# Optimization experiments

Hardware: AMD Instinct MI355X
Metric: run time of the kernel (lower is better)

Reference implementation:

```python
import jax, jax.numpy as jnp
import numpy as np

N = 50000
E = 1600000
IN_DIM = 128
OUT_DIM = 128
HEADS = 4
C = OUT_DIM // HEADS  # per-head channels = 32
EDGE_DIM = 16
NEG_SLOPE = 0.2
LN_EPS = 1e-5


def setup_inputs() -> dict:
    key = jax.random.key(0)
    ks = jax.random.split(key, 12)
    s = 1.0 / np.sqrt(IN_DIM)
    return {
        "x": jax.random.normal(ks[0], (N, IN_DIM), dtype=jnp.float32),
        "edge_index": jax.random.randint(ks[1], (2, E), 0, N, dtype=jnp.int64),
        "edge_attr": jax.random.normal(ks[2], (E, EDGE_DIM), dtype=jnp.float32),
        # GATv2Conv params
        "W_l": jax.random.normal(ks[3], (IN_DIM, HEADS * C), dtype=jnp.float32) * s,
        "b_l": jnp.zeros((HEADS * C,), dtype=jnp.float32),
        "W_r": jax.random.normal(ks[4], (IN_DIM, HEADS * C), dtype=jnp.float32) * s,
        "b_r": jnp.zeros((HEADS * C,), dtype=jnp.float32),
        "W_e": jax.random.normal(ks[5], (EDGE_DIM, HEADS * C), dtype=jnp.float32) * (1.0 / np.sqrt(EDGE_DIM)),
        "att": jax.random.normal(ks[6], (HEADS, C), dtype=jnp.float32) * (1.0 / np.sqrt(C)),
        "conv_bias": jnp.zeros((HEADS * C,), dtype=jnp.float32),
        # LayerNorm params
        "gamma": jnp.ones((OUT_DIM,), dtype=jnp.float32),
        "beta": jnp.zeros((OUT_DIM,), dtype=jnp.float32),
    }


def _gat_layer(x, edge_index, edge_attr, W_l, b_l, W_r, b_r, W_e, att, conv_bias, gamma, beta):
    src, dst = edge_index[0], edge_index[1]
    # linear projections -> [N, H, C] / [E, H, C]
    x_l = (x @ W_l + b_l).reshape(N, HEADS, C)  # source-side
    x_r = (x @ W_r + b_r).reshape(N, HEADS, C)  # target-side
    e_f = (edge_attr @ W_e).reshape(E, HEADS, C)
    # GATv2 attention logits per edge/head
    z = x_l[src] + x_r[dst] + e_f                      # [E, H, C]
    z = jnp.where(z >= 0, z, NEG_SLOPE * z)            # LeakyReLU(0.2)
    logits = jnp.einsum('ehc,hc->eh', z, att)          # [E, H]
    # segment softmax over incoming edges of each target node
    m = jax.ops.segment_max(logits, dst, num_segments=N)          # [N, H]
    m = jnp.where(jnp.isfinite(m), m, 0.0)
    ex = jnp.exp(logits - m[dst])                                  # [E, H]
    denom = jax.ops.segment_sum(ex, dst, num_segments=N)          # [N, H]
    alpha = ex / (denom[dst] + 1e-16)                              # [E, H]
    # weighted message aggregation (dropout on alpha skipped: eval mode)
    msg = x_l[src] * alpha[:, :, None]                             # [E, H, C]
    out = jax.ops.segment_sum(msg, dst, num_segments=N)           # [N, H, C]
    out = out.reshape(N, HEADS * C) + conv_bias                    # concat heads
    # LayerNorm -> ReLU -> (dropout: identity) -> residual (Identity since in==out)
    mu = jnp.mean(out, axis=-1, keepdims=True)
    var = jnp.mean(jnp.square(out - mu), axis=-1, keepdims=True)
    out = (out - mu) * jax.lax.rsqrt(var + LN_EPS) * gamma + beta
    out = jax.nn.relu(out)
    return out + x


def reference(x, edge_index, edge_attr, W_l, b_l, W_r, b_r, W_e, att, conv_bias, gamma, beta):
    return _gat_layer(x, edge_index, edge_attr, W_l, b_l, W_r, b_r, W_e, att, conv_bias, gamma, beta)
```

## Files before the change

kernel.cpp:

```cpp
#include <hip/hip_runtime.h>
#include <hip/hip_bf16.h>

#define NPB 16
#define EPB 256

__device__ __forceinline__ float b2f(__hip_bfloat16 v) { return __bfloat162float(v); }
__device__ __forceinline__ float ldf(const void* p, long i, int f32) {
    return f32 ? ((const float*)p)[i] : b2f(((const __hip_bfloat16*)p)[i]);
}
__device__ __forceinline__ float bflo(unsigned u) { union { unsigned i; float f; } v; v.i = u << 16; return v.f; }
__device__ __forceinline__ float bfhi(unsigned u) { union { unsigned i; float f; } v; v.i = u & 0xffff0000u; return v.f; }
__device__ __forceinline__ float2 ldf2(const void* p, long i2, int f32) {
    if (f32) return ((const float2*)p)[i2];
    unsigned u = ((const unsigned*)p)[i2];
    return make_float2(bflo(u), bfhi(u));
}
__device__ __forceinline__ int ldi(const int* p, long i, int i32) {
    return i32 ? p[i] : p[2 * i];
}

template <int CTRL>
__device__ __forceinline__ float dpp_add(float v) {
    int s = __builtin_amdgcn_update_dpp(0, __float_as_int(v), CTRL, 0xF, 0xF, true);
    return v + __int_as_float(s);
}

__global__ void zero_i(int* __restrict__ a, long n, int* __restrict__ dt)
{
    long i = (long)blockIdx.x * 256 + threadIdx.x;
    long stride = (long)gridDim.x * 256;
    for (; i < n; i += stride) a[i] = 0;
    if (blockIdx.x == 0 && threadIdx.x == 0 && dt) { dt[0] = 0; dt[1] = 0; }
}

__global__ void fail_stamp(float* __restrict__ out, float code)
{
    if (threadIdx.x == 0 && blockIdx.x == 0) out[0] = code;
}

__global__ void detect_kernel(const void* __restrict__ x, const int* __restrict__ ei,
                              int* __restrict__ dt, int E_)
{
    int t = threadIdx.x;
    const unsigned short* xb = (const unsigned short*)x;
    int f32 = 0;
    for (int i = t; i < 4096; i += 256) {
        int ex = (xb[i] >> 7) & 0xFF;
        if (ex > 140) f32 = 1;
    }
    if (f32) atomicOr(&dt[0], 1);
    int nz = 0;
    for (int i = t; i < 2048; i += 256) nz |= ei[2 * i + 1];
    if (nz) atomicOr(&dt[1], 1);
}

__global__ __launch_bounds__(128) void gemm_xlr(
    const void* __restrict__ x,
    const void* __restrict__ Wl, const void* __restrict__ bl,
    const void* __restrict__ Wr, const void* __restrict__ br,
    const int* __restrict__ dt,
    __hip_bfloat16* __restrict__ xl, __hip_bfloat16* __restrict__ xr, int n)
{
    __shared__ float xs[NPB][128];
    int f32 = dt[0];
    int t = threadIdx.x;
    int n0 = blockIdx.x * NPB;
    for (int j = 0; j < NPB; ++j) {
        int node = n0 + j;
        xs[j][t] = (node < n) ? ldf(x, (long)node * 128 + t, f32) : 0.f;
    }
    __syncthreads();
    float accl[NPB], accr[NPB];
#pragma unroll
    for (int j = 0; j < NPB; ++j) { accl[j] = 0.f; accr[j] = 0.f; }
    for (int k = 0; k < 128; ++k) {
        float wl = ldf(Wl, k * 128 + t, f32);
        float wr = ldf(Wr, k * 128 + t, f32);
#pragma unroll
        for (int j = 0; j < NPB; ++j) {
            float xv = xs[j][k];
            accl[j] = fmaf(xv, wl, accl[j]);
            accr[j] = fmaf(xv, wr, accr[j]);
        }
    }
    float blv = ldf(bl, t, f32);
    float brv = ldf(br, t, f32);
    for (int j = 0; j < NPB; ++j) {
        int node = n0 + j;
        if (node < n) {
            xl[(long)node * 128 + t] = __float2bfloat16(accl[j] + blv);
            xr[(long)node * 128 + t] = __float2bfloat16(accr[j] + brv);
        }
    }
}

__global__ void hist_kernel(const int* __restrict__ ei, const int* __restrict__ dt,
                            int* __restrict__ cnt, int E_, int N_)
{
    long e = (long)blockIdx.x * 256 + threadIdx.x;
    if (e >= E_) return;
    int d = ldi(ei, E_ + e, dt[1]);
    if ((unsigned)d < (unsigned)N_) atomicAdd(&cnt[d], 1);
}

__global__ __launch_bounds__(1024) void scan_kernel(
    const int* __restrict__ cnt, int* __restrict__ row_ptr, int* __restrict__ fill, int n)
{
    __shared__ int wsum[16];
    __shared__ int carry_s;
    int t = threadIdx.x; int lane = t & 63; int w = t >> 6;
    if (t == 0) { carry_s = 0; row_ptr[0] = 0; }
    __syncthreads();
    for (int base = 0; base < n; base += 1024) {
        int idx = base + t;
        int v = (idx < n) ? cnt[idx] : 0;
        int s = v;
        for (int o = 1; o < 64; o <<= 1) { int u = __shfl_up(s, o, 64); if (lane >= o) s += u; }
        if (lane == 63) wsum[w] = s;
        __syncthreads();
        int carry = carry_s;
        if (w == 0) {
            int ws = (lane < 16) ? wsum[lane] : 0;
            for (int o = 1; o < 16; o <<= 1) { int u = __shfl_up(ws, o, 64); if (lane >= o) ws += u; }
            if (lane < 16) wsum[lane] = ws;
        }
        __syncthreads();
        int woff = (w > 0) ? wsum[w - 1] : 0;
        int incl = s + woff;
        if (idx < n) { row_ptr[idx + 1] = carry + incl; fill[idx] = carry + incl - v; }
        __syncthreads();
        if (t == 0) carry_s = carry + wsum[15];
        __syncthreads();
    }
}

__global__ __launch_bounds__(256) void edge_csr(
    const int* __restrict__ ei, const int* __restrict__ dt,
    const void* __restrict__ ea, const void* __restrict__ We, const void* __restrict__ att,
    const __hip_bfloat16* __restrict__ xl, const __hip_bfloat16* __restrict__ xr,
    int* __restrict__ fill, int* __restrict__ src_sorted, float* __restrict__ lsorted,
    int E_, int N_)
{
    __shared__ int src_s[EPB], dst_s[EPB], pos_s[EPB];
    int t = threadIdx.x;
    int f32 = dt[0], i32 = dt[1];
    int wu = __builtin_amdgcn_readfirstlane(t >> 6);
    int j = t & 63;
    int h = j >> 4;

    float We0[16], We1[16];
#pragma unroll
    for (int k = 0; k < 16; ++k) {
        float2 v = ldf2(We, (long)k * 64 + j, f32);
        We0[k] = v.x; We1[k] = v.y;
    }
    float2 attv = ldf2(att, j, f32);

    long e0 = (long)blockIdx.x * EPB;
    {
        long e = e0 + t;
        if (e < E_) {
            int s = ldi(ei, e, i32);
            int d = ldi(ei, E_ + e, i32);
            src_s[t] = s; dst_s[t] = d;
            pos_s[t] = ((unsigned)d < (unsigned)N_ && (unsigned)s < (unsigned)N_)
                         ? atomicAdd(&fill[d], 1) : -1;
        } else pos_s[t] = -1;
    }
    __syncthreads();

    const unsigned* xlu = (const unsigned*)xl;
    const unsigned* xru = (const unsigned*)xr;
    for (int it = 0; it < EPB / 4; ++it) {
        int le = (it << 2) | wu;
        int pos = __builtin_amdgcn_readfirstlane(pos_s[le]);
        if (pos < 0) continue;
        int s = __builtin_amdgcn_readfirstlane(src_s[le]);
        int d = __builtin_amdgcn_readfirstlane(dst_s[le]);
        unsigned ul = (xlu + ((long)s << 6))[j];
        unsigned ur = (xru + ((long)d << 6))[j];
        long e = e0 + le;
        float a[16];
        if (f32) {
            const float4* q = (const float4*)((const float*)ea + e * 16);
            float4 q0 = q[0], q1 = q[1], q2 = q[2], q3 = q[3];
            a[0]=q0.x; a[1]=q0.y; a[2]=q0.z; a[3]=q0.w;
            a[4]=q1.x; a[5]=q1.y; a[6]=q1.z; a[7]=q1.w;
            a[8]=q2.x; a[9]=q2.y; a[10]=q2.z; a[11]=q2.w;
            a[12]=q3.x; a[13]=q3.y; a[14]=q3.z; a[15]=q3.w;
        } else {
            const uint4* q = (const uint4*)((const __hip_bfloat16*)ea + e * 16);
            uint4 q0 = q[0], q1 = q[1];
            a[0]=bflo(q0.x); a[1]=bfhi(q0.x); a[2]=bflo(q0.y); a[3]=bfhi(q0.y);
            a[4]=bflo(q0.z); a[5]=bfhi(q0.z); a[6]=bflo(q0.w); a[7]=bfhi(q0.w);
            a[8]=bflo(q1.x); a[9]=bfhi(q1.x); a[10]=bflo(q1.y); a[11]=bfhi(q1.y);
            a[12]=bflo(q1.z); a[13]=bfhi(q1.z); a[14]=bflo(q1.w); a[15]=bfhi(q1.w);
        }
        float z0 = bflo(ul) + bflo(ur);
        float z1 = bfhi(ul) + bfhi(ur);
#pragma unroll
        for (int k = 0; k < 16; ++k) {
            z0 = fmaf(a[k], We0[k], z0);
            z1 = fmaf(a[k], We1[k], z1);
        }
        z0 = fmaxf(z0, 0.2f * z0);
        z1 = fmaxf(z1, 0.2f * z1);
        float v = fmaf(z1, attv.y, z0 * attv.x);
        v = dpp_add<0xB1>(v);
        v = dpp_add<0x4E>(v);
        v = dpp_add<0x124>(v);
        v = dpp_add<0x128>(v);
        if ((j & 15) == 0) lsorted[(long)pos * 4 + h] = __expf(v);
        if (j == 0) src_sorted[pos] = s;
    }
}

__global__ __launch_bounds__(256) void node_csr(
    const int* __restrict__ row_ptr, const int* __restrict__ src_sorted,
    const float* __restrict__ lsorted, const __hip_bfloat16* __restrict__ xl,
    const void* __restrict__ cb, const void* __restrict__ gamma,
    const void* __restrict__ beta, const void* __restrict__ x,
    const int* __restrict__ dt, float* __restrict__ out, int N_)
{
    int w = threadIdx.x >> 6, j = threadIdx.x & 63;
    int n = blockIdx.x * 4 + w;
    if (n >= N_) return;
    int f32 = dt[0];
    int h = j >> 4;
    int beg = row_ptr[n], end = row_ptr[n + 1];
    float acc0 = 0.f, acc1 = 0.f, den = 0.f;
    const unsigned* xlu = (const unsigned*)xl;
    int i = beg;
    for (; i + 3 < end; i += 4) {
        int s0 = src_sorted[i],     s1 = src_sorted[i + 1];
        int s2 = src_sorted[i + 2], s3 = src_sorted[i + 3];
        float e0 = lsorted[(long)i * 4 + h];
        float e1 = lsorted[(long)(i + 1) * 4 + h];
        float e2 = lsorted[(long)(i + 2) * 4 + h];
        float e3 = lsorted[(long)(i + 3) * 4 + h];
        const unsigned* r0 = xlu + ((long)__builtin_amdgcn_readfirstlane(s0) << 6);
        const unsigned* r1 = xlu + ((long)__builtin_amdgcn_readfirstlane(s1) << 6);
        const unsigned* r2 = xlu + ((long)__builtin_amdgcn_readfirstlane(s2) << 6);
        const unsigned* r3 = xlu + ((long)__builtin_amdgcn_readfirstlane(s3) << 6);
        unsigned u0 = r0[j], u1 = r1[j], u2 = r2[j], u3 = r3[j];
        acc0 = fmaf(e0, bflo(u0), acc0); acc1 = fmaf(e0, bfhi(u0), acc1);
        acc0 = fmaf(e1, bflo(u1), acc0); acc1 = fmaf(e1, bfhi(u1), acc1);
        acc0 = fmaf(e2, bflo(u2), acc0); acc1 = fmaf(e2, bfhi(u2), acc1);
        acc0 = fmaf(e3, bflo(u3), acc0); acc1 = fmaf(e3, bfhi(u3), acc1);
        den += (e0 + e1) + (e2 + e3);
    }
    for (; i < end; ++i) {
        int s0 = src_sorted[i];
        float e0 = lsorted[(long)i * 4 + h];
        unsigned u0 = (xlu + ((long)__builtin_amdgcn_readfirstlane(s0) << 6))[j];
        acc0 = fmaf(e0, bflo(u0), acc0); acc1 = fmaf(e0, bfhi(u0), acc1);
        den += e0;
    }
    float rden = 1.f / (den + 1e-16f);
    float2 cbv = ldf2(cb, j, f32);
    float o0 = acc0 * rden + cbv.x;
    float o1 = acc1 * rden + cbv.y;

    float s = o0 + o1;
#pragma unroll
    for (int o = 1; o < 64; o <<= 1) s += __shfl_xor(s, o, 64);
    float mu = s * (1.f / 128.f);
    float d0 = o0 - mu, d1 = o1 - mu;
    float vs = d0 * d0 + d1 * d1;
#pragma unroll
    for (int o = 1; o < 64; o <<= 1) vs += __shfl_xor(vs, o, 64);
    float rs = rsqrtf(vs * (1.f / 128.f) + 1e-5f);
    float2 gv = ldf2(gamma, j, f32);
    float2 bv = ldf2(beta, j, f32);
    float2 xv = ldf2(x, (long)n * 64 + j, f32);
    float y0 = fmaxf(d0 * rs * gv.x + bv.x, 0.f) + xv.x;
    float y1 = fmaxf(d1 * rs * gv.y + bv.y, 0.f) + xv.y;
    *(float2*)(out + (long)n * 128 + 2 * j) = make_float2(y0, y1);
}

extern "C" void kernel_launch(void* const* d_in, const int* in_sizes, int n_in,
                              void* d_out, int out_size, void* d_ws, size_t ws_size,
                              hipStream_t stream) {
    const void* x     = d_in[0];
    const int*  ei    = (const int*)d_in[1];
    const void* ea    = d_in[2];
    const void* Wl    = d_in[3];
    const void* bl    = d_in[4];
    const void* Wr    = d_in[5];
    const void* br    = d_in[6];
    const void* We    = d_in[7];
    const void* att   = d_in[8];
    const void* cb    = d_in[9];
    const void* gamma = d_in[10];
    const void* beta  = d_in[11];
    float* out = (float*)d_out;

    const int N_ = in_sizes[0] / 128;
    const int E_ = in_sizes[2] / 16;

    size_t need = 0;
    auto sz = [&](size_t b) { size_t r = need; need += (b + 255) & ~(size_t)255; return r; };
    size_t o_xl   = sz((size_t)N_ * 128 * 2);
    size_t o_xr   = sz((size_t)N_ * 128 * 2);
    size_t o_cnt  = sz((size_t)N_ * 4);
    size_t o_row  = sz((size_t)(N_ + 1) * 4);
    size_t o_fill = sz((size_t)N_ * 4);
    size_t o_dt   = sz(256);
    size_t o_src  = sz((size_t)E_ * 4);
    size_t o_lsr  = sz((size_t)E_ * 16);

    if (need > ws_size) {
        fail_stamp<<<1, 64, 0, stream>>>(out, 16384.f);
        return;
    }
    char* p = (char*)d_ws;
    __hip_bfloat16* xl   = (__hip_bfloat16*)(p + o_xl);
    __hip_bfloat16* xr   = (__hip_bfloat16*)(p + o_xr);
    int*   cnt           = (int*)(p + o_cnt);
    int*   row_ptr       = (int*)(p + o_row);
    int*   fill          = (int*)(p + o_fill);
    int*   dt            = (int*)(p + o_dt);
    int*   src_sorted    = (int*)(p + o_src);
    float* lsorted       = (float*)(p + o_lsr);

    zero_i<<<256, 256, 0, stream>>>(cnt, N_, dt);
    detect_kernel<<<1, 256, 0, stream>>>(x, ei, dt, E_);
    gemm_xlr<<<(N_ + NPB - 1) / NPB, 128, 0, stream>>>(x, Wl, bl, Wr, br, dt, xl, xr, N_);
    hist_kernel<<<(E_ + 255) / 256, 256, 0, stream>>>(ei, dt, cnt, E_, N_);
    scan_kernel<<<1, 1024, 0, stream>>>(cnt, row_ptr, fill, N_);
    edge_csr<<<(E_ + EPB - 1) / EPB, 256, 0, stream>>>(ei, dt, ea, We, att, xl, xr,
                                                       fill, src_sorted, lsorted, E_, N_);
    node_csr<<<(N_ + 3) / 4, 256, 0, stream>>>(row_ptr, src_sorted, lsorted, xl,
                                               cb, gamma, beta, x, dt, out, N_);
}
```

Before: 757.8 us.

## Stage edge attributes in LDS and software-pipeline gathers in edge and node kernels

The edge kernel now loads each block's edge attributes into shared memory with coalesced loads before its loop, and prefetches the next edge's x_l/x_r rows while computing the current one. The node aggregation kernel double-buffers its 4-wide gather of source rows and logits so the next group's loads are in flight during the FMAs. The aim is to hide gather latency and cut redundant per-wavefront global loads of edge attributes. In exchange it uses 16 KB of LDS per block and more registers, which could lower occupancy, and it issues an extra dummy load of row 0 for invalid or final edges.

```diff
diff --git a/kernel.cpp b/kernel.cpp
--- a/kernel.cpp
+++ b/kernel.cpp
@@ -18,6 +18,7 @@
 __device__ __forceinline__ int ldi(const int* p, long i, int i32) {
     return i32 ? p[i] : p[2 * i];
 }
+__device__ __forceinline__ int rfl(int v) { return __builtin_amdgcn_readfirstlane(v); }
 
 template <int CTRL>
 __device__ __forceinline__ float dpp_add(float v) {
@@ -141,10 +142,11 @@
     int* __restrict__ fill, int* __restrict__ src_sorted, float* __restrict__ lsorted,
     int E_, int N_)
 {
+    __shared__ float4 ea_s4[EPB][4];
     __shared__ int src_s[EPB], dst_s[EPB], pos_s[EPB];
     int t = threadIdx.x;
     int f32 = dt[0], i32 = dt[1];
-    int wu = __builtin_amdgcn_readfirstlane(t >> 6);
+    int wu = rfl(t >> 6);
     int j = t & 63;
     int h = j >> 4;
 
@@ -157,6 +159,24 @@
     float2 attv = ldf2(att, j, f32);
 
     long e0 = (long)blockIdx.x * EPB;
+    if (f32) {
+        const float4* eg = (const float4*)ea;
+        float4* dst4 = (float4*)ea_s4;
+        for (int i = t; i < EPB * 4; i += 256) {
+            long gi = e0 * 4 + i;
+            dst4[i] = (gi < (long)E_ * 4) ? eg[gi] : make_float4(0.f, 0.f, 0.f, 0.f);
+        }
+    } else {
+        const uint4* eg = (const uint4*)ea;
+        float* eaf = (float*)ea_s4;
+        for (int i = t; i < EPB * 2; i += 256) {
+            long gi = e0 * 2 + i;
+            uint4 q = (gi < (long)E_ * 2) ? eg[gi] : make_uint4(0u, 0u, 0u, 0u);
+            float* d8 = eaf + i * 8;
+            d8[0] = bflo(q.x); d8[1] = bfhi(q.x); d8[2] = bflo(q.y); d8[3] = bfhi(q.y);
+            d8[4] = bflo(q.z); d8[5] = bfhi(q.z); d8[6] = bflo(q.w); d8[7] = bfhi(q.w);
+        }
+    }
     {
         long e = e0 + t;
         if (e < E_) {
@@ -171,38 +191,46 @@
 
     const unsigned* xlu = (const unsigned*)xl;
     const unsigned* xru = (const unsigned*)xr;
-    for (int it = 0; it < EPB / 4; ++it) {
-        int le = (it << 2) | wu;
-        int pos = __builtin_amdgcn_readfirstlane(pos_s[le]);
-        if (pos < 0) continue;
-        int s = __builtin_amdgcn_readfirstlane(src_s[le]);
-        int d = __builtin_amdgcn_readfirstlane(dst_s[le]);
-        unsigned ul = (xlu + ((long)s << 6))[j];
-        unsigned ur = (xru + ((long)d << 6))[j];
-        long e = e0 + le;
-        float a[16];
-        if (f32) {
-            const float4* q = (const float4*)((const float*)ea + e * 16);
-            float4 q0 = q[0], q1 = q[1], q2 = q[2], q3 = q[3];
-            a[0]=q0.x; a[1]=q0.y; a[2]=q0.z; a[3]=q0.w;
-            a[4]=q1.x; a[5]=q1.y; a[6]=q1.z; a[7]=q1.w;
-            a[8]=q2.x; a[9]=q2.y; a[10]=q2.z; a[11]=q2.w;
-            a[12]=q3.x; a[13]=q3.y; a[14]=q3.z; a[15]=q3.w;
-        } else {
-            const uint4* q = (const uint4*)((const __hip_bfloat16*)ea + e * 16);
-            uint4 q0 = q[0], q1 = q[1];
-            a[0]=bflo(q0.x); a[1]=bfhi(q0.x); a[2]=bflo(q0.y); a[3]=bfhi(q0.y);
-            a[4]=bflo(q0.z); a[5]=bfhi(q0.z); a[6]=bflo(q0.w); a[7]=bfhi(q0.w);
-            a[8]=bflo(q1.x); a[9]=bfhi(q1.x); a[10]=bflo(q1.y); a[11]=bfhi(q1.y);
-            a[12]=bflo(q1.z); a[13]=bfhi(q1.z); a[14]=bflo(q1.w); a[15]=bfhi(q1.w);
-        }
-        float z0 = bflo(ul) + bflo(ur);
-        float z1 = bfhi(ul) + bfhi(ur);
-#pragma unroll
-        for (int k = 0; k < 16; ++k) {
-            z0 = fmaf(a[k], We0[k], z0);
-            z1 = fmaf(a[k], We1[k], z1);
-        }
+    const int NIT = EPB / 4;
+
+    int leC = wu;
+    int posC = rfl(pos_s[leC]);
+    int sC = rfl(src_s[leC]);
+    int dC = rfl(dst_s[leC]);
+    unsigned ulC = xlu[((long)(posC >= 0 ? sC : 0) << 6) + j];
+    unsigned urC = xru[((long)(posC >= 0 ? dC : 0) << 6) + j];
+
+    for (int it = 0; it < NIT; ++it) {
+        int leN = leC + 4;
+        int posN = -1, sN = 0, dN = 0;
+        if (it + 1 < NIT) {
+            posN = rfl(pos_s[leN]);
+            sN = rfl(src_s[leN]);
+            dN = rfl(dst_s[leN]);
+        }
+        unsigned ulN = xlu[((long)(posN >= 0 ? sN : 0) << 6) + j];
+        unsigned urN = xru[((long)(posN >= 0 ? dN : 0) << 6) + j];
+
+        float4 a0 = ea_s4[leC][0], a1 = ea_s4[leC][1];
+        float4 a2 = ea_s4[leC][2], a3 = ea_s4[leC][3];
+        float z0 = bflo(ulC) + bflo(urC);
+        float z1 = bfhi(ulC) + bfhi(urC);
+        z0 = fmaf(a0.x, We0[0],  z0); z1 = fmaf(a0.x, We1[0],  z1);
+        z0 = fmaf(a0.y, We0[1],  z0); z1 = fmaf(a0.y, We1[1],  z1);
+        z0 = fmaf(a0.z, We0[2],  z0); z1 = fmaf(a0.z, We1[2],  z1);
+        z0 = fmaf(a0.w, We0[3],  z0); z1 = fmaf(a0.w, We1[3],  z1);
+        z0 = fmaf(a1.x, We0[4],  z0); z1 = fmaf(a1.x, We1[4],  z1);
+        z0 = fmaf(a1.y, We0[5],  z0); z1 = fmaf(a1.y, We1[5],  z1);
+        z0 = fmaf(a1.z, We0[6],  z0); z1 = fmaf(a1.z, We1[6],  z1);
+        z0 = fmaf(a1.w, We0[7],  z0); z1 = fmaf(a1.w, We1[7],  z1);
+        z0 = fmaf(a2.x, We0[8],  z0); z1 = fmaf(a2.x, We1[8],  z1);
+        z0 = fmaf(a2.y, We0[9],  z0); z1 = fmaf(a2.y, We1[9],  z1);
+        z0 = fmaf(a2.z, We0[10], z0); z1 = fmaf(a2.z, We1[10], z1);
+        z0 = fmaf(a2.w, We0[11], z0); z1 = fmaf(a2.w, We1[11], z1);
+        z0 = fmaf(a3.x, We0[12], z0); z1 = fmaf(a3.x, We1[12], z1);
+        z0 = fmaf(a3.y, We0[13], z0); z1 = fmaf(a3.y, We1[13], z1);
+        z0 = fmaf(a3.z, We0[14], z0); z1 = fmaf(a3.z, We1[14], z1);
+        z0 = fmaf(a3.w, We0[15], z0); z1 = fmaf(a3.w, We1[15], z1);
         z0 = fmaxf(z0, 0.2f * z0);
         z1 = fmaxf(z1, 0.2f * z1);
         float v = fmaf(z1, attv.y, z0 * attv.x);
@@ -210,8 +238,11 @@
         v = dpp_add<0x4E>(v);
         v = dpp_add<0x124>(v);
         v = dpp_add<0x128>(v);
-        if ((j & 15) == 0) lsorted[(long)pos * 4 + h] = __expf(v);
-        if (j == 0) src_sorted[pos] = s;
+        if (posC >= 0) {
+            if ((j & 15) == 0) lsorted[(long)posC * 4 + h] = __expf(v);
+            if (j == 0) src_sorted[posC] = sC;
+        }
+        leC = leN; posC = posN; sC = sN; ulC = ulN; urC = urN;
     }
 }
 
@@ -230,31 +261,57 @@
     int beg = row_ptr[n], end = row_ptr[n + 1];
     float acc0 = 0.f, acc1 = 0.f, den = 0.f;
     const unsigned* xlu = (const unsigned*)xl;
-    int i = beg;
-    for (; i + 3 < end; i += 4) {
-        int s0 = src_sorted[i],     s1 = src_sorted[i + 1];
-        int s2 = src_sorted[i + 2], s3 = src_sorted[i + 3];
-        float e0 = lsorted[(long)i * 4 + h];
-        float e1 = lsorted[(long)(i + 1) * 4 + h];
-        float e2 = lsorted[(long)(i + 2) * 4 + h];
-        float e3 = lsorted[(long)(i + 3) * 4 + h];
-        const unsigned* r0 = xlu + ((long)__builtin_amdgcn_readfirstlane(s0) << 6);
-        const unsigned* r1 = xlu + ((long)__builtin_amdgcn_readfirstlane(s1) << 6);
-        const unsigned* r2 = xlu + ((long)__builtin_amdgcn_readfirstlane(s2) << 6);
-        const unsigned* r3 = xlu + ((long)__builtin_amdgcn_readfirstlane(s3) << 6);
-        unsigned u0 = r0[j], u1 = r1[j], u2 = r2[j], u3 = r3[j];
+    int full = (end - beg) & ~3;
+    int iend = beg + full;
+    unsigned u0, u1, u2, u3;
+    float e0, e1, e2, e3;
+    if (full) {
+        int s0 = rfl(src_sorted[beg]);
+        int s1 = rfl(src_sorted[beg + 1]);
+        int s2 = rfl(src_sorted[beg + 2]);
+        int s3 = rfl(src_sorted[beg + 3]);
+        e0 = lsorted[(long)beg * 4 + h];
+        e1 = lsorted[(long)(beg + 1) * 4 + h];
+        e2 = lsorted[(long)(beg + 2) * 4 + h];
+        e3 = lsorted[(long)(beg + 3) * 4 + h];
+        u0 = xlu[((long)s0 << 6) + j]; u1 = xlu[((long)s1 << 6) + j];
+        u2 = xlu[((long)s2 << 6) + j]; u3 = xlu[((long)s3 << 6) + j];
+    }
+    for (int i = beg; i + 4 < iend; i += 4) {
+        int ix = i + 4;
+        int s0n = rfl(src_sorted[ix]);
+        int s1n = rfl(src_sorted[ix + 1]);
+        int s2n = rfl(src_sorted[ix + 2]);
+        int s3n = rfl(src_sorted[ix + 3]);
+        float e0n = lsorted[(long)ix * 4 + h];
+        float e1n = lsorted[(long)(ix + 1) * 4 + h];
+        float e2n = lsorted[(long)(ix + 2) * 4 + h];
+        float e3n = lsorted[(long)(ix + 3) * 4 + h];
+        unsigned u0n = xlu[((long)s0n << 6) + j];
+        unsigned u1n = xlu[((long)s1n << 6) + j];
+        unsigned u2n = xlu[((long)s2n << 6) + j];
+        unsigned u3n = xlu[((long)s3n << 6) + j];
         acc0 = fmaf(e0, bflo(u0), acc0); acc1 = fmaf(e0, bfhi(u0), acc1);
         acc0 = fmaf(e1, bflo(u1), acc0); acc1 = fmaf(e1, bfhi(u1), acc1);
         acc0 = fmaf(e2, bflo(u2), acc0); acc1 = fmaf(e2, bfhi(u2), acc1);
         acc0 = fmaf(e3, bflo(u3), acc0); acc1 = fmaf(e3, bfhi(u3), acc1);
         den += (e0 + e1) + (e2 + e3);
-    }
-    for (; i < end; ++i) {
-        int s0 = src_sorted[i];
-        float e0 = lsorted[(long)i * 4 + h];
-        unsigned u0 = (xlu + ((long)__builtin_amdgcn_readfirstlane(s0) << 6))[j];
+        u0 = u0n; u1 = u1n; u2 = u2n; u3 = u3n;
+        e0 = e0n; e1 = e1n; e2 = e2n; e3 = e3n;
+    }
+    if (full) {
         acc0 = fmaf(e0, bflo(u0), acc0); acc1 = fmaf(e0, bfhi(u0), acc1);
-        den += e0;
+        acc0 = fmaf(e1, bflo(u1), acc0); acc1 = fmaf(e1, bfhi(u1), acc1);
+        acc0 = fmaf(e2, bflo(u2), acc0); acc1 = fmaf(e2, bfhi(u2), acc1);
+        acc0 = fmaf(e3, bflo(u3), acc0); acc1 = fmaf(e3, bfhi(u3), acc1);
+        den += (e0 + e1) + (e2 + e3);
+    }
+    for (int i = iend; i < end; ++i) {
+        int s0 = rfl(src_sorted[i]);
+        float ee = lsorted[(long)i * 4 + h];
+        unsigned uu = xlu[((long)s0 << 6) + j];
+        acc0 = fmaf(ee, bflo(uu), acc0); acc1 = fmaf(ee, bfhi(uu), acc1);
+        den += ee;
     }
     float rden = 1.f / (den + 1e-16f);
     float2 cbv = ldf2(cb, j, f32);
```

Result: faster. 682.6 us (-9.9%).
